# Performance work log

Measured on AMD Instinct MI355X. Metric: run time of the kernel, lower is better.

## Reference

```python
import jax, jax.numpy as jnp
import numpy as np

HIDDEN_DIM = 128
BATCH, SEQ = 8, 32768


def setup_inputs() -> dict:
    key = jax.random.key(0)
    k1, k2 = jax.random.split(key)
    x = jax.random.normal(k1, (BATCH, SEQ, 2 * HIDDEN_DIM), dtype=jnp.float32)
    weight = jax.random.normal(k2, (HIDDEN_DIM, HIDDEN_DIM), dtype=jnp.float32) * 0.02
    return {"x": x, "weight": weight}


def reference(x, weight):
    # RevNet-style additive coupling:
    #   y1 = x1
    #   y2 = x2 + Hamilton(x1, W)   (bilinear map realized as x1 @ W)
    x1, x2 = jnp.split(x, 2, axis=-1)            # each [B, S, D]
    h = jnp.einsum("bsd,de->bse", x1, weight)    # tiled Hamilton product
    y2 = x2 + h
    return jnp.concatenate([x1, y2], axis=-1)    # [B, S, 2D]
```

## Files before the change

### kernel.cpp

```cpp
#include <hip/hip_runtime.h>
#include <hip/hip_bf16.h>

typedef __bf16 bf16x8 __attribute__((ext_vector_type(8)));
typedef float  f32x4  __attribute__((ext_vector_type(4)));

#define HD  128
#define ROW 256

__global__ __launch_bounds__(256, 4)
void revnet_mfma(const float* __restrict__ x, const float* __restrict__ w,
                 float* __restrict__ out, int num_chunks) {
    __shared__ __attribute__((aligned(16))) __bf16 ldsB[2048 * 8];

    const int tid    = threadIdx.x;
    const int lane   = tid & 63;
    const int wave   = tid >> 6;
    const int lane15 = lane & 15;
    const int quad   = lane >> 4;

    #pragma unroll
    for (int i = 0; i < 8; ++i) {
        int s  = i * 256 + tid;
        int sl = s & 63;
        int t  = s >> 6;
        int ks = t & 3;
        int nt = t >> 2;
        int k0 = ks * 32 + (sl >> 4) * 8;
        int n  = nt * 16 + (sl & 15);
        bf16x8 frag;
        #pragma unroll
        for (int j = 0; j < 8; ++j)
            frag[j] = (__bf16)w[(k0 + j) * HD + n];
        *(bf16x8*)&ldsB[s * 8] = frag;
    }
    __syncthreads();

    for (int c = blockIdx.x; c < num_chunks; c += gridDim.x) {
        const int m0   = c * 64 + wave * 16;
        const int arow = m0 + lane15;
        const float* __restrict__ xr = x   + (size_t)arow * ROW;
        float*       __restrict__ yr = out + (size_t)arow * ROW;

        bf16x8 afrag[4];
        #pragma unroll
        for (int ks = 0; ks < 4; ++ks) {
            const int k0 = ks * 32 + quad * 8;
            f32x4 v0 = *(const f32x4*)(xr + k0);
            f32x4 v1 = *(const f32x4*)(xr + k0 + 4);
            *(f32x4*)(yr + k0)     = v0;
            *(f32x4*)(yr + k0 + 4) = v1;
            #pragma unroll
            for (int j = 0; j < 4; ++j) {
                afrag[ks][j]     = (__bf16)v0[j];
                afrag[ks][j + 4] = (__bf16)v1[j];
            }
        }

        f32x4 acc[8];
        #pragma unroll
        for (int nt = 0; nt < 8; ++nt) acc[nt] = (f32x4){0.f, 0.f, 0.f, 0.f};

        #pragma unroll
        for (int ks = 0; ks < 4; ++ks) {
            #pragma unroll
            for (int nt = 0; nt < 8; ++nt) {
                bf16x8 bfrag = *(const bf16x8*)&ldsB[((nt * 4 + ks) * 64 + lane) * 8];
                acc[nt] = __builtin_amdgcn_mfma_f32_16x16x32_bf16(
                              afrag[ks], bfrag, acc[nt], 0, 0, 0);
            }
        }

        #pragma unroll
        for (int nt = 0; nt < 8; ++nt) {
            const int col = HD + nt * 16 + lane15;
            #pragma unroll
            for (int r = 0; r < 4; ++r) {
                const size_t idx = (size_t)(m0 + quad * 4 + r) * ROW + col;
                out[idx] = x[idx] + acc[nt][r];
            }
        }
    }
}

extern "C" void kernel_launch(void* const* d_in, const int* in_sizes, int n_in,
                              void* d_out, int out_size, void* d_ws, size_t ws_size,
                              hipStream_t stream) {
    const float* x   = (const float*)d_in[0];
    const float* w   = (const float*)d_in[1];
    float*       out = (float*)d_out;

    const int rows       = out_size / ROW;
    const int num_chunks = rows / 64;
    int grid = num_chunks < 1024 ? num_chunks : 1024;

    revnet_mfma<<<dim3(grid), dim3(256), 0, stream>>>(x, w, out, num_chunks);
}
```

Baseline: 524.9 us.

## Coalesce row loads and stores via swizzled per-wave LDS staging

Each wave now loads its 16 full rows with fully coalesced 16-byte-per-lane reads and keeps them in registers. The x1 half is converted to bf16 and staged in a swizzled per-wave LDS tile, which supplies the MFMA A fragments; the MFMA operands are swapped so the output comes out transposed. The result h goes back through LDS as bf16 and is added to x2 in the register copy before fully coalesced row stores. This removes the scattered per-lane-row accesses and the second global read of x2. In exchange, h is rounded to bf16 before the add, which adds some precision loss, and the grid is reduced to 768 blocks.

```diff
diff --git a/kernel.cpp b/kernel.cpp
--- a/kernel.cpp
+++ b/kernel.cpp
@@ -1,22 +1,26 @@
 #include <hip/hip_runtime.h>
 #include <hip/hip_bf16.h>
 
+typedef __bf16 bf16x4 __attribute__((ext_vector_type(4)));
 typedef __bf16 bf16x8 __attribute__((ext_vector_type(8)));
 typedef float  f32x4  __attribute__((ext_vector_type(4)));
 
-#define HD  128
-#define ROW 256
+#define HD   128
+#define ROW  256
+#define TROW 256
 
 __global__ __launch_bounds__(256, 4)
 void revnet_mfma(const float* __restrict__ x, const float* __restrict__ w,
                  float* __restrict__ out, int num_chunks) {
-    __shared__ __attribute__((aligned(16))) __bf16 ldsB[2048 * 8];
+    __shared__ __attribute__((aligned(16))) __bf16 ldsW[2048 * 8];
+    __shared__ __attribute__((aligned(16))) __bf16 ldsT[4][16 * 128];
 
     const int tid    = threadIdx.x;
     const int lane   = tid & 63;
     const int wave   = tid >> 6;
     const int lane15 = lane & 15;
     const int quad   = lane >> 4;
+    const int l31    = lane & 31;
 
     #pragma unroll
     for (int i = 0; i < 8; ++i) {
@@ -31,28 +35,29 @@
         #pragma unroll
         for (int j = 0; j < 8; ++j)
             frag[j] = (__bf16)w[(k0 + j) * HD + n];
-        *(bf16x8*)&ldsB[s * 8] = frag;
+        *(bf16x8*)&ldsW[s * 8] = frag;
     }
     __syncthreads();
 
+    char* T = (char*)&ldsT[wave][0];
+
     for (int c = blockIdx.x; c < num_chunks; c += gridDim.x) {
-        const int m0   = c * 64 + wave * 16;
-        const int arow = m0 + lane15;
-        const float* __restrict__ xr = x   + (size_t)arow * ROW;
-        float*       __restrict__ yr = out + (size_t)arow * ROW;
+        const int m0 = c * 64 + wave * 16;
+        const float* __restrict__ xr = x   + (size_t)m0 * ROW;
+        float*       __restrict__ yr = out + (size_t)m0 * ROW;
 
-        bf16x8 afrag[4];
+        f32x4 r[16];
         #pragma unroll
-        for (int ks = 0; ks < 4; ++ks) {
-            const int k0 = ks * 32 + quad * 8;
-            f32x4 v0 = *(const f32x4*)(xr + k0);
-            f32x4 v1 = *(const f32x4*)(xr + k0 + 4);
-            *(f32x4*)(yr + k0)     = v0;
-            *(f32x4*)(yr + k0 + 4) = v1;
+        for (int i = 0; i < 16; ++i)
+            r[i] = *(const f32x4*)(xr + i * ROW + 4 * lane);
+
+        if (lane < 32) {
             #pragma unroll
-            for (int j = 0; j < 4; ++j) {
-                afrag[ks][j]     = (__bf16)v0[j];
-                afrag[ks][j + 4] = (__bf16)v1[j];
+            for (int i = 0; i < 16; ++i) {
+                bf16x4 b;
+                b[0] = (__bf16)r[i][0]; b[1] = (__bf16)r[i][1];
+                b[2] = (__bf16)r[i][2]; b[3] = (__bf16)r[i][3];
+                *(bf16x4*)(T + i * TROW + ((l31 * 8) ^ ((i & 7) << 4))) = b;
             }
         }
 
@@ -62,22 +67,34 @@
 
         #pragma unroll
         for (int ks = 0; ks < 4; ++ks) {
+            bf16x8 af = *(const bf16x8*)(T + lane15 * TROW +
+                          ((ks * 64 + quad * 16) ^ ((lane15 & 7) << 4)));
             #pragma unroll
             for (int nt = 0; nt < 8; ++nt) {
-                bf16x8 bfrag = *(const bf16x8*)&ldsB[((nt * 4 + ks) * 64 + lane) * 8];
+                bf16x8 bfrag = *(const bf16x8*)&ldsW[((nt * 4 + ks) * 64 + lane) * 8];
                 acc[nt] = __builtin_amdgcn_mfma_f32_16x16x32_bf16(
-                              afrag[ks], bfrag, acc[nt], 0, 0, 0);
+                              bfrag, af, acc[nt], 0, 0, 0);
             }
         }
 
         #pragma unroll
         for (int nt = 0; nt < 8; ++nt) {
-            const int col = HD + nt * 16 + lane15;
-            #pragma unroll
-            for (int r = 0; r < 4; ++r) {
-                const size_t idx = (size_t)(m0 + quad * 4 + r) * ROW + col;
-                out[idx] = x[idx] + acc[nt][r];
+            bf16x4 hb;
+            hb[0] = (__bf16)acc[nt][0]; hb[1] = (__bf16)acc[nt][1];
+            hb[2] = (__bf16)acc[nt][2]; hb[3] = (__bf16)acc[nt][3];
+            *(bf16x4*)(T + lane15 * TROW +
+                       ((nt * 32 + quad * 8) ^ ((lane15 & 7) << 4))) = hb;
+        }
+
+        #pragma unroll
+        for (int i = 0; i < 16; ++i) {
+            bf16x4 hb = *(const bf16x4*)(T + i * TROW + ((l31 * 8) ^ ((i & 7) << 4)));
+            f32x4 v = r[i];
+            if (lane >= 32) {
+                v[0] += (float)hb[0]; v[1] += (float)hb[1];
+                v[2] += (float)hb[2]; v[3] += (float)hb[3];
             }
+            *(f32x4*)(yr + i * ROW + 4 * lane) = v;
         }
     }
 }
@@ -91,7 +108,7 @@
 
     const int rows       = out_size / ROW;
     const int num_chunks = rows / 64;
-    int grid = num_chunks < 1024 ? num_chunks : 1024;
+    int grid = num_chunks < 768 ? num_chunks : 768;
 
     revnet_mfma<<<dim3(grid), dim3(256), 0, stream>>>(x, w, out, num_chunks);
 }
```

Result: faster. 437.2 us (-16.7%).
